# Optimization experiments

Hardware: AMD Instinct MI355X
Metric: run time of the kernel (lower is better)

Reference implementation:

```python
import jax, jax.numpy as jnp
import numpy as np

HIDDEN = 2048
N_HEADS = 32
N_KV_HEADS = 8
HEAD_DIM = HIDDEN // N_HEADS  # 64
KV_DIM = N_KV_HEADS * HEAD_DIM  # 512


def setup_inputs() -> dict:
    key = jax.random.key(0)
    ks = jax.random.split(key, 9)
    s = 1.0 / np.sqrt(HIDDEN)
    x = jax.random.normal(ks[0], (2, 2048, HIDDEN), dtype=jnp.float32)
    wq = jax.random.uniform(ks[1], (HIDDEN, HIDDEN), jnp.float32, -s, s)
    bq = jax.random.uniform(ks[2], (HIDDEN,), jnp.float32, -s, s)
    wk = jax.random.uniform(ks[3], (KV_DIM, HIDDEN), jnp.float32, -s, s)
    bk = jax.random.uniform(ks[4], (KV_DIM,), jnp.float32, -s, s)
    wv = jax.random.uniform(ks[5], (KV_DIM, HIDDEN), jnp.float32, -s, s)
    bv = jax.random.uniform(ks[6], (KV_DIM,), jnp.float32, -s, s)
    wo = jax.random.uniform(ks[7], (HIDDEN, HIDDEN), jnp.float32, -s, s)
    bo = jax.random.uniform(ks[8], (HIDDEN,), jnp.float32, -s, s)
    return {"x": x, "wq": wq, "bq": bq, "wk": wk, "bk": bk,
            "wv": wv, "bv": bv, "wo": wo, "bo": bo}


def reference(x, wq, bq, wk, bk, wv, bv, wo, bo):
    B, S, _ = x.shape
    group = N_HEADS // N_KV_HEADS  # 4
    # projections (torch Linear: x @ W.T + b)
    q = (x @ wq.T + bq).reshape(B, S, N_HEADS, HEAD_DIM).transpose(0, 2, 1, 3)      # [B,H,S,D]
    k = (x @ wk.T + bk).reshape(B, S, N_KV_HEADS, HEAD_DIM).transpose(0, 2, 1, 3)   # [B,Hk,S,D]
    v = (x @ wv.T + bv).reshape(B, S, N_KV_HEADS, HEAD_DIM).transpose(0, 2, 1, 3)
    # repeat_interleave KV heads to match query heads
    k = jnp.repeat(k, group, axis=1)  # [B,H,S,D]
    v = jnp.repeat(v, group, axis=1)
    scale = 1.0 / np.sqrt(HEAD_DIM).astype(np.float32)
    attn = jnp.einsum('bhqd,bhkd->bhqk', q, k) * scale  # [B,H,S,S]
    score = jax.nn.softmax(attn, axis=-1)
    out = jnp.einsum('bhqk,bhkd->bhqd', score, v)       # [B,H,S,D]
    out = out.transpose(0, 2, 1, 3).reshape(B, S, HIDDEN)
    return out @ wo.T + bo
```

## Files before the change

kernel.cpp:

```cpp
#include <hip/hip_runtime.h>

typedef __attribute__((ext_vector_type(8))) short bf16x8;
typedef __attribute__((ext_vector_type(4))) float f32x4;

__device__ __forceinline__ float b2f(short s) {
  union { unsigned u; float f; } c;
  c.u = ((unsigned)(unsigned short)s) << 16;
  return c.f;
}
__device__ __forceinline__ short f2b(float f) {
  union { unsigned u; float f; } c;
  c.f = f;
  unsigned r = (c.u + 0x7FFFu + ((c.u >> 16) & 1u)) >> 16;
  return (short)r;
}
__device__ __forceinline__ short f2b_fast(float f) {
  union { unsigned u; float f; } c;
  c.f = f;
  return (short)((c.u + 0x8000u) >> 16);
}

__device__ __forceinline__ void async16(const void* g, void* l) {
  __builtin_amdgcn_global_load_lds(
      (const __attribute__((address_space(1))) unsigned*)g,
      (__attribute__((address_space(3))) unsigned*)l, 16, 0, 0);
}

__global__ __launch_bounds__(256)
void f32_to_bf16(const float* __restrict__ src, short* __restrict__ dst, int n) {
  int i = (blockIdx.x * blockDim.x + threadIdx.x) * 4;
  if (i < n) {
    float4 v = *(const float4*)(src + i);
    short4 o;
    o.x = f2b(v.x); o.y = f2b(v.y); o.z = f2b(v.z); o.w = f2b(v.w);
    *(short4*)(dst + i) = o;
  }
}

template <bool F32OUT>
__global__ __launch_bounds__(256)
void gemm_bt_bias(const short* __restrict__ A, const short* __restrict__ Bw,
                  const float* __restrict__ bias, void* __restrict__ Cv,
                  int M, int N, int K) {
  __shared__ short lsA[128 * 32];
  __shared__ short lsB[128 * 32];
  const int tid  = threadIdx.x;
  const int wave = tid >> 6, lane = tid & 63;
  const int quad = lane >> 4, lrow = lane & 15;
  const int m0 = blockIdx.y * 128, n0 = blockIdx.x * 128;
  const int wm = (wave >> 1) * 64, wn = (wave & 1) * 64;

  f32x4 zero = {0.f, 0.f, 0.f, 0.f};
  f32x4 acc[4][4];
#pragma unroll
  for (int i = 0; i < 4; i++)
#pragma unroll
    for (int j = 0; j < 4; j++) acc[i][j] = zero;

  const int r0 = tid >> 2, c0 = (tid & 3) * 8;
  const short* Ab  = A  + (size_t)(m0 + r0) * K + c0;
  const short* Ab2 = A  + (size_t)(m0 + r0 + 64) * K + c0;
  const short* Bb  = Bw + (size_t)(n0 + r0) * K + c0;
  const short* Bb2 = Bw + (size_t)(n0 + r0 + 64) * K + c0;

  for (int k0 = 0; k0 < K; k0 += 32) {
    async16(Ab  + k0, lsA + tid * 8);
    async16(Ab2 + k0, lsA + (tid + 256) * 8);
    async16(Bb  + k0, lsB + tid * 8);
    async16(Bb2 + k0, lsB + (tid + 256) * 8);
    __syncthreads();

    bf16x8 af[4], bfr[4];
#pragma unroll
    for (int i = 0; i < 4; i++)
      af[i] = *(const bf16x8*)(lsA + (wm + i * 16 + lrow) * 32 + quad * 8);
#pragma unroll
    for (int j = 0; j < 4; j++)
      bfr[j] = *(const bf16x8*)(lsB + (wn + j * 16 + lrow) * 32 + quad * 8);
#pragma unroll
    for (int i = 0; i < 4; i++)
#pragma unroll
      for (int j = 0; j < 4; j++)
        acc[i][j] = __builtin_amdgcn_mfma_f32_16x16x32_bf16(af[i], bfr[j], acc[i][j], 0, 0, 0);
    __syncthreads();
  }

#pragma unroll
  for (int j = 0; j < 4; j++) {
    const int col = n0 + wn + j * 16 + lrow;
    const float bv = bias[col];
#pragma unroll
    for (int i = 0; i < 4; i++) {
      const int rowb = m0 + wm + i * 16 + quad * 4;
#pragma unroll
      for (int r = 0; r < 4; r++) {
        const float val = acc[i][j][r] + bv;
        if (F32OUT)
          ((float*)Cv)[(size_t)(rowb + r) * N + col] = val;
        else
          ((short*)Cv)[(size_t)(rowb + r) * N + col] = f2b(val);
      }
    }
  }
}

__global__ __launch_bounds__(256)
void gemm_qkv(const short* __restrict__ A, const short* __restrict__ Bw,
              const float* __restrict__ bq, const float* __restrict__ bk,
              const float* __restrict__ bv,
              short* __restrict__ Qo, short* __restrict__ Ko, short* __restrict__ Vo) {
  const int K = 2048;
  __shared__ short lsA[128 * 32];
  __shared__ short lsB[128 * 32];
  const int tid  = threadIdx.x;
  const int wave = tid >> 6, lane = tid & 63;
  const int quad = lane >> 4, lrow = lane & 15;
  const int m0 = blockIdx.y * 128, n0 = blockIdx.x * 128;
  const int wm = (wave >> 1) * 64, wn = (wave & 1) * 64;

  f32x4 zero = {0.f, 0.f, 0.f, 0.f};
  f32x4 acc[4][4];
#pragma unroll
  for (int i = 0; i < 4; i++)
#pragma unroll
    for (int j = 0; j < 4; j++) acc[i][j] = zero;

  const int r0 = tid >> 2, c0 = (tid & 3) * 8;
  const short* Ab  = A  + (size_t)(m0 + r0) * K + c0;
  const short* Ab2 = A  + (size_t)(m0 + r0 + 64) * K + c0;
  const short* Bb  = Bw + (size_t)(n0 + r0) * K + c0;
  const short* Bb2 = Bw + (size_t)(n0 + r0 + 64) * K + c0;

  for (int k0 = 0; k0 < K; k0 += 32) {
    async16(Ab  + k0, lsA + tid * 8);
    async16(Ab2 + k0, lsA + (tid + 256) * 8);
    async16(Bb  + k0, lsB + tid * 8);
    async16(Bb2 + k0, lsB + (tid + 256) * 8);
    __syncthreads();

    bf16x8 af[4], bfr[4];
#pragma unroll
    for (int i = 0; i < 4; i++)
      af[i] = *(const bf16x8*)(lsA + (wm + i * 16 + lrow) * 32 + quad * 8);
#pragma unroll
    for (int j = 0; j < 4; j++)
      bfr[j] = *(const bf16x8*)(lsB + (wn + j * 16 + lrow) * 32 + quad * 8);
#pragma unroll
    for (int i = 0; i < 4; i++)
#pragma unroll
      for (int j = 0; j < 4; j++)
        acc[i][j] = __builtin_amdgcn_mfma_f32_16x16x32_bf16(af[i], bfr[j], acc[i][j], 0, 0, 0);
    __syncthreads();
  }

  short* base; int stride, coff; const float* bias;
  if (n0 < 2048)      { base = Qo; stride = 2048; bias = bq; coff = 0; }
  else if (n0 < 2560) { base = Ko; stride = 512;  bias = bk; coff = 2048; }
  else                { base = Vo; stride = 512;  bias = bv; coff = 2560; }

#pragma unroll
  for (int j = 0; j < 4; j++) {
    const int lc = n0 + wn + j * 16 + lrow - coff;
    const float bvv = bias[lc];
#pragma unroll
    for (int i = 0; i < 4; i++) {
      const int rowb = m0 + wm + i * 16 + quad * 4;
#pragma unroll
      for (int r = 0; r < 4; r++)
        base[(size_t)(rowb + r) * stride + lc] = f2b(acc[i][j][r] + bvv);
    }
  }
}

#define S_LEN 2048
#define HID   2048
#define KVD   512
#define ST    72

__global__ __launch_bounds__(256)
void gqa_flash(const short* __restrict__ Q, const short* __restrict__ Kb,
               const short* __restrict__ Vb, short* __restrict__ O) {
  __shared__ __align__(16) short lsQP[4 * 32 * ST];
  __shared__ __align__(16) short lsK[64 * ST];
  __shared__ __align__(16) short lsVt[80 * ST];

  const int tid  = threadIdx.x;
  const int wave = tid >> 6, lane = tid & 63;
  const int quad = lane >> 4, lrow = lane & 15;
  const int by = blockIdx.y, b = by >> 3, kvh = by & 7;
  const int h = kvh * 4 + wave;
  const int q0 = blockIdx.x * 32;

  for (int c = tid; c < 1024; c += 256) {
    const int head = c >> 8, qr = (c >> 3) & 31, ch = (c & 7) * 8;
    bf16x8 v = *(const bf16x8*)(Q + (size_t)(b * S_LEN + q0 + qr) * HID +
                                (kvh * 4 + head) * 64 + ch);
    bf16x8 w;
#pragma unroll
    for (int jj = 0; jj < 8; jj++) w[jj] = f2b(b2f(v[jj]) * 0.125f);
    *(bf16x8*)(lsQP + head * (32 * ST) + qr * ST + ch) = w;
  }
  for (int c = tid; c < 16 * 36; c += 256) {
    const int rr = c / 36, dw = c - rr * 36;
    ((unsigned*)lsVt)[(64 + rr) * 36 + dw] = (rr == 0) ? 0x3F803F80u : 0u;
  }
  __syncthreads();

  bf16x8 aq[2][2];
#pragma unroll
  for (int i = 0; i < 2; i++)
#pragma unroll
    for (int hh = 0; hh < 2; hh++)
      aq[i][hh] = *(const bf16x8*)(lsQP + wave * (32 * ST) +
                                   (i * 16 + lrow) * ST + hh * 32 + quad * 8);
  bf16x8 bv4a = *(const bf16x8*)(lsVt + (64 + lrow) * ST + quad * 8);
  bf16x8 bv4b = *(const bf16x8*)(lsVt + (64 + lrow) * ST + 32 + quad * 8);

  f32x4 zero = {0.f, 0.f, 0.f, 0.f};
  f32x4 o[2][5];
#pragma unroll
  for (int i = 0; i < 2; i++)
#pragma unroll
    for (int j = 0; j < 5; j++) o[i][j] = zero;

  const short* Kp = Kb + (size_t)b * S_LEN * KVD + kvh * 64;
  const short* Vp = Vb + (size_t)b * S_LEN * KVD + kvh * 64;

  const int keyA = tid >> 3, chK = (tid & 7) * 8;
  const int kpV = tid & 31, dcV = (tid >> 5) * 8;

  bf16x8 kf0 = *(const bf16x8*)(Kp + (size_t)keyA * KVD + chK);
  bf16x8 kf1 = *(const bf16x8*)(Kp + (size_t)(keyA + 32) * KVD + chK);
  bf16x8 vf0 = *(const bf16x8*)(Vp + (size_t)(2 * kpV) * KVD + dcV);
  bf16x8 vf1 = *(const bf16x8*)(Vp + (size_t)(2 * kpV + 1) * KVD + dcV);

  const int cW = 16 * (quad >> 1);
  const int cR = 16 * ((lrow >> 3) & 1);
  short* Pw = lsQP + wave * (32 * ST);

  for (int k0 = 0; k0 < S_LEN; k0 += 64) {
    *(bf16x8*)(lsK + keyA * ST + chK) = kf0;
    *(bf16x8*)(lsK + (keyA + 32) * ST + chK) = kf1;
#pragma unroll
    for (int jj = 0; jj < 8; jj++) {
      unsigned pk = (unsigned)(unsigned short)vf0[jj] |
                    ((unsigned)(unsigned short)vf1[jj] << 16);
      *(unsigned*)(lsVt + (dcV + jj) * ST + 2 * kpV) = pk;
    }
    __syncthreads();

    const int kn = (k0 + 64) & (S_LEN - 1);
    kf0 = *(const bf16x8*)(Kp + (size_t)(kn + keyA) * KVD + chK);
    kf1 = *(const bf16x8*)(Kp + (size_t)(kn + keyA + 32) * KVD + chK);
    vf0 = *(const bf16x8*)(Vp + (size_t)(kn + 2 * kpV) * KVD + dcV);
    vf1 = *(const bf16x8*)(Vp + (size_t)(kn + 2 * kpV + 1) * KVD + dcV);

    f32x4 s[2][4];
#pragma unroll
    for (int j = 0; j < 4; j++) {
      bf16x8 bk0 = *(const bf16x8*)(lsK + (j * 16 + lrow) * ST + quad * 8);
      bf16x8 bk1 = *(const bf16x8*)(lsK + (j * 16 + lrow) * ST + 32 + quad * 8);
#pragma unroll
      for (int i = 0; i < 2; i++) {
        f32x4 t = zero;
        t = __builtin_amdgcn_mfma_f32_16x16x32_bf16(aq[i][0], bk0, t, 0, 0, 0);
        t = __builtin_amdgcn_mfma_f32_16x16x32_bf16(aq[i][1], bk1, t, 0, 0, 0);
        s[i][j] = t;
      }
    }

#pragma unroll
    for (int i = 0; i < 2; i++)
#pragma unroll
      for (int j = 0; j < 4; j++)
#pragma unroll
        for (int r = 0; r < 4; r++)
          Pw[(i * 16 + quad * 4 + r) * ST + ((j * 16 + lrow) ^ cW)] =
              f2b_fast(__expf(s[i][j][r]));

    bf16x8 ap[2][2];
#pragma unroll
    for (int i = 0; i < 2; i++)
#pragma unroll
      for (int hh = 0; hh < 2; hh++)
        ap[i][hh] = *(const bf16x8*)(Pw + (i * 16 + lrow) * ST +
                                     ((hh * 32 + quad * 8) ^ cR));
#pragma unroll
    for (int jd = 0; jd < 4; jd++) {
      bf16x8 bv0 = *(const bf16x8*)(lsVt + (jd * 16 + lrow) * ST + quad * 8);
      bf16x8 bv1 = *(const bf16x8*)(lsVt + (jd * 16 + lrow) * ST + 32 + quad * 8);
#pragma unroll
      for (int i = 0; i < 2; i++) {
        o[i][jd] = __builtin_amdgcn_mfma_f32_16x16x32_bf16(ap[i][0], bv0, o[i][jd], 0, 0, 0);
        o[i][jd] = __builtin_amdgcn_mfma_f32_16x16x32_bf16(ap[i][1], bv1, o[i][jd], 0, 0, 0);
      }
    }
#pragma unroll
    for (int i = 0; i < 2; i++) {
      o[i][4] = __builtin_amdgcn_mfma_f32_16x16x32_bf16(ap[i][0], bv4a, o[i][4], 0, 0, 0);
      o[i][4] = __builtin_amdgcn_mfma_f32_16x16x32_bf16(ap[i][1], bv4b, o[i][4], 0, 0, 0);
    }
    __syncthreads();
  }

#pragma unroll
  for (int i = 0; i < 2; i++)
#pragma unroll
    for (int r = 0; r < 4; r++) {
      const float l = __shfl(o[i][4][r], quad << 4);
      const float rl = 1.0f / l;
      const int row = q0 + i * 16 + quad * 4 + r;
#pragma unroll
      for (int jd = 0; jd < 4; jd++) {
        const int col = h * 64 + jd * 16 + lrow;
        O[(size_t)(b * S_LEN + row) * HID + col] = f2b(o[i][jd][r] * rl);
      }
    }
}

extern "C" void kernel_launch(void* const* d_in, const int* in_sizes, int n_in,
                              void* d_out, int out_size, void* d_ws, size_t ws_size,
                              hipStream_t stream) {
  const float* x  = (const float*)d_in[0];
  const float* wq = (const float*)d_in[1];
  const float* bq = (const float*)d_in[2];
  const float* wk = (const float*)d_in[3];
  const float* bk = (const float*)d_in[4];
  const float* wv = (const float*)d_in[5];
  const float* bv = (const float*)d_in[6];
  const float* wo = (const float*)d_in[7];
  const float* bo = (const float*)d_in[8];
  float* out = (float*)d_out;

  short* xb  = (short*)d_ws;
  short* wqb = xb  + (size_t)4096 * 2048;
  short* wkb = wqb + (size_t)2048 * 2048;
  short* wvb = wkb + (size_t)512 * 2048;
  short* wob = wvb + (size_t)512 * 2048;
  short* Qb  = wob + (size_t)2048 * 2048;
  short* Kb  = Qb  + (size_t)4096 * 2048;
  short* Vb  = Kb  + (size_t)4096 * 512;
  short* AO  = Vb  + (size_t)4096 * 512;

  dim3 blk(256);
  f32_to_bf16<<<4096 * 2048 / 1024, blk, 0, stream>>>(x,  xb,  4096 * 2048);
  f32_to_bf16<<<2048 * 2048 / 1024, blk, 0, stream>>>(wq, wqb, 2048 * 2048);
  f32_to_bf16<<< 512 * 2048 / 1024, blk, 0, stream>>>(wk, wkb, 512 * 2048);
  f32_to_bf16<<< 512 * 2048 / 1024, blk, 0, stream>>>(wv, wvb, 512 * 2048);
  f32_to_bf16<<<2048 * 2048 / 1024, blk, 0, stream>>>(wo, wob, 2048 * 2048);

  gemm_qkv<<<dim3(3072 / 128, 4096 / 128), blk, 0, stream>>>(xb, wqb, bq, bk, bv, Qb, Kb, Vb);
  gqa_flash<<<dim3(2048 / 32, 16), blk, 0, stream>>>(Qb, Kb, Vb, AO);
  gemm_bt_bias<true><<<dim3(2048 / 128, 4096 / 128), blk, 0, stream>>>(AO, wob, bo, out, 4096, 2048, 2048);
}
```

Before: 379.6 us.

## Double-buffer K/V via async LDS loads, emit transposed V from QKV GEMM

The QKV GEMM now writes V already transposed (d-major), so the attention kernel can stream K and V tiles straight into swizzled, double-buffered LDS with async global-to-LDS loads instead of register staging and a scalar transpose. The prefetch of the next tile overlaps with the current tile's compute. Other changes: exp is done as exp2 with log2e folded into the Q scale, the row-sum column comes from a register constant instead of LDS, launch bounds hint 3 blocks per CU, and the five fp32-to-bf16 conversion launches are merged into one. The transposed V store writes short4 with a large stride, which may hurt the GEMM epilogue, and double buffering raises LDS use.

New measurement: 387.6 us. 2.1% more time.

```diff
diff --git a/kernel.cpp b/kernel.cpp
--- a/kernel.cpp
+++ b/kernel.cpp
@@ -27,14 +27,20 @@
 }
 
 __global__ __launch_bounds__(256)
-void f32_to_bf16(const float* __restrict__ src, short* __restrict__ dst, int n) {
-  int i = (blockIdx.x * blockDim.x + threadIdx.x) * 4;
-  if (i < n) {
-    float4 v = *(const float4*)(src + i);
-    short4 o;
-    o.x = f2b(v.x); o.y = f2b(v.y); o.z = f2b(v.z); o.w = f2b(v.w);
-    *(short4*)(dst + i) = o;
-  }
+void f32_to_bf16_all(const float* __restrict__ s0, const float* __restrict__ s1,
+                     const float* __restrict__ s2, const float* __restrict__ s3,
+                     const float* __restrict__ s4, short* __restrict__ dst) {
+  const long long gi = (long long)blockIdx.x * 1024 + threadIdx.x * 4;
+  const float* src; long long off;
+  if (gi < 8388608)       { src = s0; off = 0; }
+  else if (gi < 12582912) { src = s1; off = 8388608; }
+  else if (gi < 13631488) { src = s2; off = 12582912; }
+  else if (gi < 14680064) { src = s3; off = 13631488; }
+  else                    { src = s4; off = 14680064; }
+  float4 v = *(const float4*)(src + (gi - off));
+  short4 o;
+  o.x = f2b(v.x); o.y = f2b(v.y); o.z = f2b(v.z); o.w = f2b(v.w);
+  *(short4*)(dst + gi) = o;
 }
 
 template <bool F32OUT>
@@ -108,7 +114,7 @@
 void gemm_qkv(const short* __restrict__ A, const short* __restrict__ Bw,
               const float* __restrict__ bq, const float* __restrict__ bk,
               const float* __restrict__ bv,
-              short* __restrict__ Qo, short* __restrict__ Ko, short* __restrict__ Vo) {
+              short* __restrict__ Qo, short* __restrict__ Ko, short* __restrict__ Vt) {
   const int K = 2048;
   __shared__ short lsA[128 * 32];
   __shared__ short lsB[128 * 32];
@@ -153,21 +159,37 @@
     __syncthreads();
   }
 
-  short* base; int stride, coff; const float* bias;
-  if (n0 < 2048)      { base = Qo; stride = 2048; bias = bq; coff = 0; }
-  else if (n0 < 2560) { base = Ko; stride = 512;  bias = bk; coff = 2048; }
-  else                { base = Vo; stride = 512;  bias = bv; coff = 2560; }
-
-#pragma unroll
-  for (int j = 0; j < 4; j++) {
-    const int lc = n0 + wn + j * 16 + lrow - coff;
-    const float bvv = bias[lc];
-#pragma unroll
-    for (int i = 0; i < 4; i++) {
-      const int rowb = m0 + wm + i * 16 + quad * 4;
-#pragma unroll
-      for (int r = 0; r < 4; r++)
-        base[(size_t)(rowb + r) * stride + lc] = f2b(acc[i][j][r] + bvv);
+  if (n0 < 2560) {
+    short* base; int stride, coff; const float* bias;
+    if (n0 < 2048) { base = Qo; stride = 2048; bias = bq; coff = 0; }
+    else           { base = Ko; stride = 512;  bias = bk; coff = 2048; }
+#pragma unroll
+    for (int j = 0; j < 4; j++) {
+      const int lc = n0 + wn + j * 16 + lrow - coff;
+      const float bvv = bias[lc];
+#pragma unroll
+      for (int i = 0; i < 4; i++) {
+        const int rowb = m0 + wm + i * 16 + quad * 4;
+#pragma unroll
+        for (int r = 0; r < 4; r++)
+          base[(size_t)(rowb + r) * stride + lc] = f2b(acc[i][j][r] + bvv);
+      }
+    }
+  } else {
+#pragma unroll
+    for (int j = 0; j < 4; j++) {
+      const int lc = n0 + wn + j * 16 + lrow - 2560;
+      const float bvv = bv[lc];
+#pragma unroll
+      for (int i = 0; i < 4; i++) {
+        const int rowb = m0 + wm + i * 16 + quad * 4;
+        short4 pk;
+        pk.x = f2b(acc[i][j][0] + bvv);
+        pk.y = f2b(acc[i][j][1] + bvv);
+        pk.z = f2b(acc[i][j][2] + bvv);
+        pk.w = f2b(acc[i][j][3] + bvv);
+        *(short4*)(Vt + (size_t)lc * 4096 + rowb) = pk;
+      }
     }
   }
 }
@@ -177,12 +199,12 @@
 #define KVD   512
 #define ST    72
 
-__global__ __launch_bounds__(256)
+__global__ __launch_bounds__(256, 3)
 void gqa_flash(const short* __restrict__ Q, const short* __restrict__ Kb,
-               const short* __restrict__ Vb, short* __restrict__ O) {
+               const short* __restrict__ VtG, short* __restrict__ O) {
   __shared__ __align__(16) short lsQP[4 * 32 * ST];
-  __shared__ __align__(16) short lsK[64 * ST];
-  __shared__ __align__(16) short lsVt[80 * ST];
+  __shared__ __align__(16) short lsK[2][64 * 64];
+  __shared__ __align__(16) short lsV[2][64 * 64];
 
   const int tid  = threadIdx.x;
   const int wave = tid >> 6, lane = tid & 63;
@@ -191,19 +213,26 @@
   const int h = kvh * 4 + wave;
   const int q0 = blockIdx.x * 32;
 
+  const float QS = 0.125f * 1.44269504f;
   for (int c = tid; c < 1024; c += 256) {
     const int head = c >> 8, qr = (c >> 3) & 31, ch = (c & 7) * 8;
     bf16x8 v = *(const bf16x8*)(Q + (size_t)(b * S_LEN + q0 + qr) * HID +
                                 (kvh * 4 + head) * 64 + ch);
     bf16x8 w;
 #pragma unroll
-    for (int jj = 0; jj < 8; jj++) w[jj] = f2b(b2f(v[jj]) * 0.125f);
+    for (int jj = 0; jj < 8; jj++) w[jj] = f2b(b2f(v[jj]) * QS);
     *(bf16x8*)(lsQP + head * (32 * ST) + qr * ST + ch) = w;
   }
-  for (int c = tid; c < 16 * 36; c += 256) {
-    const int rr = c / 36, dw = c - rr * 36;
-    ((unsigned*)lsVt)[(64 + rr) * 36 + dw] = (rr == 0) ? 0x3F803F80u : 0u;
-  }
+
+  const int srow = tid >> 3;
+  const int swc  = ((tid & 7) ^ (srow & 7)) * 8;
+  const short* Kp = Kb  + (size_t)b * S_LEN * KVD + kvh * 64;
+  const short* Vp = VtG + (size_t)(kvh * 64) * 4096 + b * 2048;
+
+  async16(Kp + (size_t)srow * KVD + swc,        lsK[0] + tid * 8);
+  async16(Kp + (size_t)(srow + 32) * KVD + swc, lsK[0] + (tid + 256) * 8);
+  async16(Vp + (size_t)srow * 4096 + swc,       lsV[0] + tid * 8);
+  async16(Vp + (size_t)(srow + 32) * 4096 + swc, lsV[0] + (tid + 256) * 8);
   __syncthreads();
 
   bf16x8 aq[2][2];
@@ -213,8 +242,9 @@
     for (int hh = 0; hh < 2; hh++)
       aq[i][hh] = *(const bf16x8*)(lsQP + wave * (32 * ST) +
                                    (i * 16 + lrow) * ST + hh * 32 + quad * 8);
-  bf16x8 bv4a = *(const bf16x8*)(lsVt + (64 + lrow) * ST + quad * 8);
-  bf16x8 bv4b = *(const bf16x8*)(lsVt + (64 + lrow) * ST + 32 + quad * 8);
+
+  const short onev = (lrow == 0) ? (short)0x3F80 : (short)0;
+  const bf16x8 bones = {onev, onev, onev, onev, onev, onev, onev, onev};
 
   f32x4 zero = {0.f, 0.f, 0.f, 0.f};
   f32x4 o[2][5];
@@ -222,44 +252,29 @@
   for (int i = 0; i < 2; i++)
 #pragma unroll
     for (int j = 0; j < 5; j++) o[i][j] = zero;
-
-  const short* Kp = Kb + (size_t)b * S_LEN * KVD + kvh * 64;
-  const short* Vp = Vb + (size_t)b * S_LEN * KVD + kvh * 64;
-
-  const int keyA = tid >> 3, chK = (tid & 7) * 8;
-  const int kpV = tid & 31, dcV = (tid >> 5) * 8;
-
-  bf16x8 kf0 = *(const bf16x8*)(Kp + (size_t)keyA * KVD + chK);
-  bf16x8 kf1 = *(const bf16x8*)(Kp + (size_t)(keyA + 32) * KVD + chK);
-  bf16x8 vf0 = *(const bf16x8*)(Vp + (size_t)(2 * kpV) * KVD + dcV);
-  bf16x8 vf1 = *(const bf16x8*)(Vp + (size_t)(2 * kpV + 1) * KVD + dcV);
 
   const int cW = 16 * (quad >> 1);
   const int cR = 16 * ((lrow >> 3) & 1);
   short* Pw = lsQP + wave * (32 * ST);
 
-  for (int k0 = 0; k0 < S_LEN; k0 += 64) {
-    *(bf16x8*)(lsK + keyA * ST + chK) = kf0;
-    *(bf16x8*)(lsK + (keyA + 32) * ST + chK) = kf1;
-#pragma unroll
-    for (int jj = 0; jj < 8; jj++) {
-      unsigned pk = (unsigned)(unsigned short)vf0[jj] |
-                    ((unsigned)(unsigned short)vf1[jj] << 16);
-      *(unsigned*)(lsVt + (dcV + jj) * ST + 2 * kpV) = pk;
-    }
-    __syncthreads();
-
-    const int kn = (k0 + 64) & (S_LEN - 1);
-    kf0 = *(const bf16x8*)(Kp + (size_t)(kn + keyA) * KVD + chK);
-    kf1 = *(const bf16x8*)(Kp + (size_t)(kn + keyA + 32) * KVD + chK);
-    vf0 = *(const bf16x8*)(Vp + (size_t)(kn + 2 * kpV) * KVD + dcV);
-    vf1 = *(const bf16x8*)(Vp + (size_t)(kn + 2 * kpV + 1) * KVD + dcV);
+  int p = 0;
+  for (int it = 0; it < S_LEN / 64; ++it) {
+    const int kn = ((it + 1) & (S_LEN / 64 - 1)) * 64;
+    async16(Kp + (size_t)(kn + srow) * KVD + swc,        lsK[p ^ 1] + tid * 8);
+    async16(Kp + (size_t)(kn + srow + 32) * KVD + swc,   lsK[p ^ 1] + (tid + 256) * 8);
+    async16(Vp + (size_t)srow * 4096 + kn + swc,         lsV[p ^ 1] + tid * 8);
+    async16(Vp + (size_t)(srow + 32) * 4096 + kn + swc,  lsV[p ^ 1] + (tid + 256) * 8);
+
+    const short* Kt = lsK[p];
+    const short* Vt = lsV[p];
 
     f32x4 s[2][4];
 #pragma unroll
     for (int j = 0; j < 4; j++) {
-      bf16x8 bk0 = *(const bf16x8*)(lsK + (j * 16 + lrow) * ST + quad * 8);
-      bf16x8 bk1 = *(const bf16x8*)(lsK + (j * 16 + lrow) * ST + 32 + quad * 8);
+      const int kr = j * 16 + lrow;
+      const int cs = (quad ^ (kr & 7)) * 8;
+      bf16x8 bk0 = *(const bf16x8*)(Kt + kr * 64 + cs);
+      bf16x8 bk1 = *(const bf16x8*)(Kt + kr * 64 + (cs ^ 32));
 #pragma unroll
       for (int i = 0; i < 2; i++) {
         f32x4 t = zero;
@@ -276,7 +291,7 @@
 #pragma unroll
         for (int r = 0; r < 4; r++)
           Pw[(i * 16 + quad * 4 + r) * ST + ((j * 16 + lrow) ^ cW)] =
-              f2b_fast(__expf(s[i][j][r]));
+              f2b_fast(__builtin_exp2f(s[i][j][r]));
 
     bf16x8 ap[2][2];
 #pragma unroll
@@ -287,8 +302,10 @@
                                      ((hh * 32 + quad * 8) ^ cR));
 #pragma unroll
     for (int jd = 0; jd < 4; jd++) {
-      bf16x8 bv0 = *(const bf16x8*)(lsVt + (jd * 16 + lrow) * ST + quad * 8);
-      bf16x8 bv1 = *(const bf16x8*)(lsVt + (jd * 16 + lrow) * ST + 32 + quad * 8);
+      const int dr = jd * 16 + lrow;
+      const int cs = (quad ^ (dr & 7)) * 8;
+      bf16x8 bv0 = *(const bf16x8*)(Vt + dr * 64 + cs);
+      bf16x8 bv1 = *(const bf16x8*)(Vt + dr * 64 + (cs ^ 32));
 #pragma unroll
       for (int i = 0; i < 2; i++) {
         o[i][jd] = __builtin_amdgcn_mfma_f32_16x16x32_bf16(ap[i][0], bv0, o[i][jd], 0, 0, 0);
@@ -297,10 +314,12 @@
     }
 #pragma unroll
     for (int i = 0; i < 2; i++) {
-      o[i][4] = __builtin_amdgcn_mfma_f32_16x16x32_bf16(ap[i][0], bv4a, o[i][4], 0, 0, 0);
-      o[i][4] = __builtin_amdgcn_mfma_f32_16x16x32_bf16(ap[i][1], bv4b, o[i][4], 0, 0, 0);
-    }
-    __syncthreads();
+      o[i][4] = __builtin_amdgcn_mfma_f32_16x16x32_bf16(ap[i][0], bones, o[i][4], 0, 0, 0);
+      o[i][4] = __builtin_amdgcn_mfma_f32_16x16x32_bf16(ap[i][1], bones, o[i][4], 0, 0, 0);
+    }
+
+    __syncthreads();
+    p ^= 1;
   }
 
 #pragma unroll
@@ -334,22 +353,16 @@
 
   short* xb  = (short*)d_ws;
   short* wqb = xb  + (size_t)4096 * 2048;
-  short* wkb = wqb + (size_t)2048 * 2048;
-  short* wvb = wkb + (size_t)512 * 2048;
-  short* wob = wvb + (size_t)512 * 2048;
+  short* wob = wqb + (size_t)3072 * 2048;
   short* Qb  = wob + (size_t)2048 * 2048;
   short* Kb  = Qb  + (size_t)4096 * 2048;
-  short* Vb  = Kb  + (size_t)4096 * 512;
-  short* AO  = Vb  + (size_t)4096 * 512;
+  short* Vt  = Kb  + (size_t)4096 * 512;
+  short* AO  = Vt  + (size_t)512 * 4096;
 
   dim3 blk(256);
-  f32_to_bf16<<<4096 * 2048 / 1024, blk, 0, stream>>>(x,  xb,  4096 * 2048);
-  f32_to_bf16<<<2048 * 2048 / 1024, blk, 0, stream>>>(wq, wqb, 2048 * 2048);
-  f32_to_bf16<<< 512 * 2048 / 1024, blk, 0, stream>>>(wk, wkb, 512 * 2048);
-  f32_to_bf16<<< 512 * 2048 / 1024, blk, 0, stream>>>(wv, wvb, 512 * 2048);
-  f32_to_bf16<<<2048 * 2048 / 1024, blk, 0, stream>>>(wo, wob, 2048 * 2048);
-
-  gemm_qkv<<<dim3(3072 / 128, 4096 / 128), blk, 0, stream>>>(xb, wqb, bq, bk, bv, Qb, Kb, Vb);
-  gqa_flash<<<dim3(2048 / 32, 16), blk, 0, stream>>>(Qb, Kb, Vb, AO);
+  f32_to_bf16_all<<<18432, blk, 0, stream>>>(x, wq, wk, wv, wo, xb);
+
+  gemm_qkv<<<dim3(3072 / 128, 4096 / 128), blk, 0, stream>>>(xb, wqb, bq, bk, bv, Qb, Kb, Vt);
+  gqa_flash<<<dim3(2048 / 32, 16), blk, 0, stream>>>(Qb, Kb, Vt, AO);
   gemm_bt_bias<true><<<dim3(2048 / 128, 4096 / 128), blk, 0, stream>>>(AO, wob, bo, out, 4096, 2048, 2048);
 }
```
